# Performance work log

Measured on AMD Instinct MI355X. Metric: run time of the kernel, lower is better.

## Reference

```python
import jax, jax.numpy as jnp
import numpy as np

TAU = 5.0
ENTROPY_REG = 0.0  # entropy branch disabled (matches init kwargs)
NEG_INF = -1.0e9
NORM_EPS = 1e-12   # F.normalize eps
COS_EPS = 1e-8     # F.cosine_similarity eps


def _l2norm(x):
    n = jnp.sqrt(jnp.sum(x * x, axis=-1, keepdims=True))
    return x / jnp.maximum(n, NORM_EPS)


def setup_inputs() -> dict:
    key = jax.random.key(0)
    k1, k2, k3 = jax.random.split(key, 3)
    B, T, D = 8, 2048, 512
    pred_tokens = jax.random.normal(k1, (B, T, D), dtype=jnp.float32)
    text_tokens = jax.random.normal(k2, (B, T, D), dtype=jnp.float32)
    text_pad_mask = jax.random.randint(k3, (B, T), 0, 2).astype(jnp.bool_)  # True = PAD
    return {"pred_tokens": pred_tokens, "text_tokens": text_tokens, "text_pad_mask": text_pad_mask}


def reference(pred_tokens, text_tokens, text_pad_mask):
    B, Tp, D = pred_tokens.shape
    Tt = text_tokens.shape[1]
    T = min(Tp, Tt)
    P = _l2norm(pred_tokens[:, :T, :])            # [B,T,D]
    E = _l2norm(text_tokens[:, :T, :])            # [B,T,D]
    valid = ~text_pad_mask[:, :T]                 # [B,T] True = valid column

    S = jnp.einsum('btd,bsd->bts', P, E)          # [B,T,T]
    S = jnp.where(valid[:, None, :], S, NEG_INF)
    A = jax.nn.softmax(S * TAU, axis=-1)          # [B,T,T]
    E_hat = jnp.einsum('bts,bsd->btd', A, E)      # [B,T,D]

    # cosine similarity with eps-clamped norms (F.cosine_similarity semantics)
    dot = jnp.sum(P * E_hat, axis=-1)             # [B,T]
    pn = jnp.maximum(jnp.sqrt(jnp.sum(P * P, axis=-1)), COS_EPS)
    en = jnp.maximum(jnp.sqrt(jnp.sum(E_hat * E_hat, axis=-1)), COS_EPS)
    cos = dot / (pn * en)                         # [B,T]

    # row_has_valid: per-batch 'any valid column', broadcast over rows
    row_valid = jnp.broadcast_to(jnp.any(valid, axis=-1, keepdims=True), cos.shape)
    w = row_valid.astype(cos.dtype)
    cnt = jnp.sum(w)
    loss_sel = jnp.sum(w * (1.0 - cos)) / jnp.maximum(cnt, 1.0)
    loss = jnp.where(cnt > 0, loss_sel, jnp.zeros((), cos.dtype))
    tas = jnp.where(cnt > 0, 1.0 - jax.lax.stop_gradient(loss), loss)
    return (loss, tas)
```

## Files before the change

kernel.cpp:

```cpp
#include <hip/hip_runtime.h>
#include <cstdint>

typedef float f32x4 __attribute__((ext_vector_type(4)));
typedef long longx2 __attribute__((ext_vector_type(2)));
typedef unsigned char u8;
typedef unsigned short u16;
typedef unsigned int u32;
typedef unsigned long long u64;

#define B_N 8
#define T_N 2048
#define D_N 512
#define TAU 5.0f
#define NROW (B_N * T_N)
#define K1E 7.213475204444817f
#define K2E 1.4426950408889634f

__device__ __forceinline__ void gload_lds16(const u8* g, u8* l) {
  __builtin_amdgcn_global_load_lds(
      (const __attribute__((address_space(1))) u32*)g,
      (__attribute__((address_space(3))) u32*)l, 16, 0, 0);
}

__device__ __forceinline__ u32 pk4_fp8(float a, float b, float c, float d) {
  int w = __builtin_amdgcn_cvt_pk_fp8_f32(a, b, 0, 0);
  w = __builtin_amdgcn_cvt_pk_fp8_f32(c, d, w, 1);
  return (u32)w;
}

__device__ __forceinline__ u16 f2bf16(float x) {
  u32 u = __builtin_bit_cast(u32, x);
  u32 r = u + 0x7fffu + ((u >> 16) & 1u);
  return (u16)(r >> 16);
}
__device__ __forceinline__ float bf2f(u16 v) {
  u32 u = ((u32)v) << 16;
  return __builtin_bit_cast(float, u);
}

__global__ void kprep(const float* __restrict__ text,
                      u8* __restrict__ EF, u8* __restrict__ ET) {
  __shared__ u8 tile[32][528];
  int b = blockIdx.y, t = blockIdx.x;
  int tr = threadIdx.x;
  int row = tr >> 3, seg = tr & 7;
  const float* src = text + ((size_t)b * T_N + t * 32 + row) * D_N + seg * 64;
  float4 v[16];
  float ss = 0.f;
#pragma unroll
  for (int j = 0; j < 16; ++j) {
    v[j] = *(const float4*)(src + j * 4);
    ss += v[j].x*v[j].x + v[j].y*v[j].y + v[j].z*v[j].z + v[j].w*v[j].w;
  }
  ss += __shfl_xor(ss, 1); ss += __shfl_xor(ss, 2); ss += __shfl_xor(ss, 4);
  float inv = 1.f / fmaxf(sqrtf(ss), 1e-12f);
  u32 w[16];
#pragma unroll
  for (int j = 0; j < 16; ++j)
    w[j] = pk4_fp8(v[j].x*inv, v[j].y*inv, v[j].z*inv, v[j].w*inv);
  uint4* ldst = (uint4*)&tile[row][seg * 64];
#pragma unroll
  for (int j = 0; j < 4; ++j)
    ldst[j] = make_uint4(w[4*j], w[4*j+1], w[4*j+2], w[4*j+3]);
  __syncthreads();
  size_t tbase = ((size_t)(b * 64 + t)) << 14;
  {
    int j = tr >> 5, tok = tr & 31;
    u32 acc[16];
#pragma unroll
    for (int g2 = 0; g2 < 4; ++g2)
#pragma unroll
      for (int h = 0; h < 2; ++h) {
        uint2 vv = *(const uint2*)&tile[tok][j*64 + h*32 + g2*8];
        acc[g2*4 + h*2] = vv.x; acc[g2*4 + h*2 + 1] = vv.y;
      }
    uint4* dst = (uint4*)(EF + tbase + tr * 64);
#pragma unroll
    for (int q = 0; q < 4; ++q)
      dst[q] = make_uint4(acc[4*q], acc[4*q+1], acc[4*q+2], acc[4*q+3]);
  }
  {
    int m = tr >> 4, g2 = (tr >> 2) & 3, c0 = (tr & 3) * 4;
    u32 acc[16];
#pragma unroll
    for (int ci = 0; ci < 4; ++ci)
#pragma unroll
      for (int h = 0; h < 2; ++h) {
        int c = c0 + ci, n = 2*m + h;
        u32 lo = 0, hi = 0;
#pragma unroll
        for (int e = 0; e < 4; ++e) lo |= (u32)tile[g2*4 + e][n*16 + c] << (8*e);
#pragma unroll
        for (int e = 0; e < 4; ++e) hi |= (u32)tile[16 + g2*4 + e][n*16 + c] << (8*e);
        acc[ci*4 + h*2] = lo; acc[ci*4 + h*2 + 1] = hi;
      }
    uint4* dst = (uint4*)(ET + tbase + tr * 64);
#pragma unroll
    for (int q = 0; q < 4; ++q)
      dst[q] = make_uint4(acc[4*q], acc[4*q+1], acc[4*q+2], acc[4*q+3]);
  }
}

__launch_bounds__(256, 2)
__global__ void kflash(const float* __restrict__ pred,
                       const u8* __restrict__ EF, const u8* __restrict__ ET,
                       const int* __restrict__ mask,
                       u16* __restrict__ Opart, float* __restrict__ Lpart) {
  int b = blockIdx.x & 7;
  int rem = blockIdx.x >> 3;
  int rb = rem & 31, h = rem >> 5;
  int wid = threadIdx.x >> 6, lane = threadIdx.x & 63;
  int g = lane >> 4, c = lane & 15;
  int row0 = rb * 64 + wid * 16;
  int t0 = h * 32;

  __shared__ u64 mbits[32];
  __shared__ __align__(16) u8 els[2][16384];
  __shared__ __align__(16) u8 etls[2][16384];

  const u8* EFb = EF + (((size_t)(b * 64)) << 14) + (lane << 4);
  const u8* ETb = ET + (((size_t)(b * 64)) << 14) + (lane << 4);

  auto stage = [&](int buf, int t) {
    size_t tb = ((size_t)t) << 14;
#pragma unroll
    for (int j = 0; j < 4; ++j) {
      int ch = j * 4 + wid;
      gload_lds16(EFb + tb + (ch << 10), &els[buf][ch << 10]);
    }
#pragma unroll
    for (int j = 0; j < 4; ++j) {
      int ch = j * 4 + wid;
      gload_lds16(ETb + tb + (ch << 10), &etls[buf][ch << 10]);
    }
  };

  for (int chunk = wid; chunk < 32; chunk += 4) {
    int col = chunk * 64 + lane;
    u64 bal = __ballot(mask[b * T_N + col] == 0);
    if (lane == 0) mbits[chunk] = bal;
  }

  stage(0, t0);

  long pf[16];
  {
    int prow = row0 + c;
    const float* pr = pred + ((size_t)(b * T_N) + prow) * D_N;
    float ss = 0.f;
#pragma unroll
    for (int kk = 0; kk < 16; ++kk) {
      float4 v0 = *(const float4*)(pr + kk * 32 + g * 8);
      float4 v1 = *(const float4*)(pr + kk * 32 + g * 8 + 4);
      ss += v0.x*v0.x + v0.y*v0.y + v0.z*v0.z + v0.w*v0.w
          + v1.x*v1.x + v1.y*v1.y + v1.z*v1.z + v1.w*v1.w;
    }
    ss += __shfl_xor(ss, 16);
    ss += __shfl_xor(ss, 32);
    float inv = 1.f / fmaxf(sqrtf(ss), 1e-12f);
#pragma unroll
    for (int kk = 0; kk < 16; ++kk) {
      float4 v0 = *(const float4*)(pr + kk * 32 + g * 8);
      float4 v1 = *(const float4*)(pr + kk * 32 + g * 8 + 4);
      u32 lo = pk4_fp8(v0.x*inv, v0.y*inv, v0.z*inv, v0.w*inv);
      u32 hi = pk4_fp8(v1.x*inv, v1.y*inv, v1.z*inv, v1.w*inv);
      pf[kk] = (long)(((u64)hi << 32) | lo);
    }
  }

  __syncthreads();

  f32x4 zero = {0.f, 0.f, 0.f, 0.f};
  f32x4 eh[32];
#pragma unroll
  for (int n = 0; n < 32; ++n) eh[n] = zero;
  float lsum = 0.f;

  const int sb_off = c * 64 + g * 16;
  const int pv_off = g * 256 + c * 16;

#pragma unroll 1
  for (int tt = 0; tt < 32; ++tt) {
    int t = t0 + tt;
    int cur = tt & 1;
    if (tt + 1 < 32) stage(cur ^ 1, t + 1);
    int c0 = t * 32;

    f32x4 ta0 = zero, tb0 = zero, ta1 = zero, tb1 = zero;
    const u8* el = &els[cur][0];
    __builtin_amdgcn_s_setprio(1);
#pragma unroll
    for (int j = 0; j < 8; ++j) {
      longx2 b0 = *(const longx2*)(el + j * 2048 + sb_off);
      longx2 b1 = *(const longx2*)(el + j * 2048 + 1024 + sb_off);
      ta0 = __builtin_amdgcn_mfma_f32_16x16x32_fp8_fp8(b0[0], pf[2*j],   ta0, 0, 0, 0);
      tb0 = __builtin_amdgcn_mfma_f32_16x16x32_fp8_fp8(b0[1], pf[2*j+1], tb0, 0, 0, 0);
      ta1 = __builtin_amdgcn_mfma_f32_16x16x32_fp8_fp8(b1[0], pf[2*j],   ta1, 0, 0, 0);
      tb1 = __builtin_amdgcn_mfma_f32_16x16x32_fp8_fp8(b1[1], pf[2*j+1], tb1, 0, 0, 0);
    }
    __builtin_amdgcn_s_setprio(0);
    f32x4 st0 = ta0 + tb0, st1 = ta1 + tb1;

    u64 mw = mbits[c0 >> 6];
    u32 sh0 = (c0 & 63) + g * 4;
    u32 bits0 = (u32)(mw >> sh0) & 0xf;
    u32 bits1 = (u32)(mw >> (sh0 + 16)) & 0xf;
    float p0[4], p1[4];
#pragma unroll
    for (int r = 0; r < 4; ++r) {
      p0[r] = (bits0 >> r) & 1 ? __builtin_exp2f(fmaf(K1E, st0[r], -K2E)) : 0.f;
      p1[r] = (bits1 >> r) & 1 ? __builtin_exp2f(fmaf(K1E, st1[r], -K2E)) : 0.f;
      lsum += p0[r] + p1[r];
    }
    u32 lo = pk4_fp8(p0[0], p0[1], p0[2], p0[3]);
    u32 hi = pk4_fp8(p1[0], p1[1], p1[2], p1[3]);
    long af = (long)(((u64)hi << 32) | lo);

    const u8* et = &etls[cur][0];
    __builtin_amdgcn_s_setprio(1);
#pragma unroll
    for (int m = 0; m < 16; ++m) {
      longx2 bv = *(const longx2*)(et + m * 1024 + pv_off);
      eh[2*m]   = __builtin_amdgcn_mfma_f32_16x16x32_fp8_fp8(af, bv[0], eh[2*m],   0, 0, 0);
      eh[2*m+1] = __builtin_amdgcn_mfma_f32_16x16x32_fp8_fp8(af, bv[1], eh[2*m+1], 0, 0, 0);
    }
    __builtin_amdgcn_s_setprio(0);
    __syncthreads();
  }

  lsum += __shfl_xor(lsum, 16);
  lsum += __shfl_xor(lsum, 32);
  u16* OP = Opart + (size_t)h * ((size_t)NROW * D_N);
#pragma unroll
  for (int r = 0; r < 4; ++r) {
    int brow = b * T_N + row0 + g * 4 + r;
    u16* orow = OP + (size_t)brow * D_N + c;
#pragma unroll
    for (int n = 0; n < 32; ++n) orow[n * 16] = f2bf16(eh[n][r]);
  }
  if (g == 0) {
    Lpart[h * NROW + b * T_N + row0 + c] = lsum;
  }
}

__global__ void kcomb(const float* __restrict__ pred, const u16* __restrict__ Opart,
                      const float* __restrict__ Lpart,
                      float* __restrict__ pl, float* __restrict__ pw) {
  __shared__ float sl[8], swv[8];
  int tr = threadIdx.x;
  int row = blockIdx.x * 8 + (tr >> 5);
  int ln = tr & 31;
  float l = Lpart[row] + Lpart[NROW + row];
  const float* pr = pred + (size_t)row * D_N + ln * 16;
  const u16* o0 = Opart + (size_t)row * D_N + ln * 16;
  const u16* o1 = o0 + (size_t)NROW * D_N;
  float dot = 0.f, e2 = 0.f, pn2 = 0.f;
#pragma unroll
  for (int q = 0; q < 2; ++q) {
    uint4 a0 = *(const uint4*)(o0 + q * 8);
    uint4 a1 = *(const uint4*)(o1 + q * 8);
    u32 w0[4] = {a0.x, a0.y, a0.z, a0.w};
    u32 w1[4] = {a1.x, a1.y, a1.z, a1.w};
    float4 p0 = *(const float4*)(pr + q * 8);
    float4 p1 = *(const float4*)(pr + q * 8 + 4);
    float pp[8] = {p0.x, p0.y, p0.z, p0.w, p1.x, p1.y, p1.z, p1.w};
#pragma unroll
    for (int j = 0; j < 8; ++j) {
      float f0 = bf2f((u16)((w0[j >> 1] >> ((j & 1) * 16)) & 0xffff));
      float f1 = bf2f((u16)((w1[j >> 1] >> ((j & 1) * 16)) & 0xffff));
      float ev = f0 + f1;
      dot += pp[j] * ev;
      e2 += ev * ev;
      pn2 += pp[j] * pp[j];
    }
  }
#pragma unroll
  for (int msk = 16; msk >= 1; msk >>= 1) {
    dot += __shfl_xor(dot, msk);
    e2 += __shfl_xor(e2, msk);
    pn2 += __shfl_xor(pn2, msk);
  }
  if (ln == 0) {
    float w = (l > 0.f) ? 1.f : 0.f;
    float pn = fmaxf(sqrtf(pn2), 1e-12f);
    float denom = pn * fmaxf(sqrtf(e2), 1e-8f * l);
    float cosv = (l > 0.f) ? dot / denom : 0.f;
    sl[tr >> 5] = w * (1.f - cosv);
    swv[tr >> 5] = w;
  }
  __syncthreads();
  if (tr == 0) {
    float a = 0.f, b2 = 0.f;
#pragma unroll
    for (int i = 0; i < 8; ++i) { a += sl[i]; b2 += swv[i]; }
    pl[blockIdx.x] = a;
    pw[blockIdx.x] = b2;
  }
}

__global__ void kreduce(const float* __restrict__ pl, const float* __restrict__ pw,
                        float* __restrict__ out) {
  __shared__ float sm[256], sw[256];
  float s = 0.f, w = 0.f;
  for (int i = threadIdx.x; i < NROW / 8; i += 256) { s += pl[i]; w += pw[i]; }
  sm[threadIdx.x] = s; sw[threadIdx.x] = w;
  __syncthreads();
#pragma unroll
  for (int st = 128; st >= 1; st >>= 1) {
    if ((int)threadIdx.x < st) {
      sm[threadIdx.x] += sm[threadIdx.x + st];
      sw[threadIdx.x] += sw[threadIdx.x + st];
    }
    __syncthreads();
  }
  if (threadIdx.x == 0) {
    float cnt = sw[0];
    float loss = (cnt > 0.f) ? sm[0] / fmaxf(cnt, 1.f) : 0.f;
    out[0] = loss;
    out[1] = (cnt > 0.f) ? 1.f - loss : 0.f;
  }
}

extern "C" void kernel_launch(void* const* d_in, const int* in_sizes, int n_in,
                              void* d_out, int out_size, void* d_ws, size_t ws_size,
                              hipStream_t stream) {
  const float* pred = (const float*)d_in[0];
  const float* text = (const float*)d_in[1];
  const int* mask = (const int*)d_in[2];
  char* ws = (char*)d_ws;
  const size_t EB8 = (size_t)B_N * T_N * D_N;
  const size_t OB = (size_t)NROW * D_N * 2;
  u8* EF = (u8*)ws;
  u8* ET = (u8*)(ws + EB8);
  u16* Opart = (u16*)(ws + 2 * EB8);
  float* Lpart = (float*)(ws + 2 * EB8 + 2 * OB);
  float* pl = (float*)(ws + 2 * EB8 + 2 * OB + 131072);
  float* pw = (float*)(ws + 2 * EB8 + 2 * OB + 131072 + 16384);
  float* out = (float*)d_out;

  kprep<<<dim3(64, 8), dim3(256), 0, stream>>>(text, EF, ET);
  kflash<<<dim3(512), dim3(256), 0, stream>>>(pred, EF, ET, mask, Opart, Lpart);
  kcomb<<<dim3(NROW / 8), dim3(256), 0, stream>>>(pred, Opart, Lpart, pl, pw);
  kreduce<<<dim3(1), dim3(256), 0, stream>>>(pl, pw, out);
}
```

Measured before the change: 106.8 us.

## Load E fragments directly from global and software-pipeline S computation one tile ahead

The QK-side E tiles are no longer staged through LDS. Each lane reads its fp8 fragment directly from global memory in an MFMA-ready layout, which halves LDS footprint and staging traffic. The S=PE^T MFMAs for tile t+1 are issued before the exp/PV work of tile t, so that global load latency is overlapped. The ET staging is reordered to prefetch two tiles ahead after the barrier. The change risks exposed global-load latency and extra registers for the carried S values, which could lower occupancy.

```diff
diff --git a/kernel.cpp b/kernel.cpp
--- a/kernel.cpp
+++ b/kernel.cpp
@@ -115,19 +115,16 @@
   int t0 = h * 32;
 
   __shared__ u64 mbits[32];
-  __shared__ __align__(16) u8 els[2][16384];
   __shared__ __align__(16) u8 etls[2][16384];
 
-  const u8* EFb = EF + (((size_t)(b * 64)) << 14) + (lane << 4);
+  const int sb_off = c * 64 + g * 16;
+  const int pv_off = g * 256 + c * 16;
+
+  const u8* EFl = EF + (((size_t)(b * 64 + t0)) << 14) + sb_off;
   const u8* ETb = ET + (((size_t)(b * 64)) << 14) + (lane << 4);
 
   auto stage = [&](int buf, int t) {
     size_t tb = ((size_t)t) << 14;
-#pragma unroll
-    for (int j = 0; j < 4; ++j) {
-      int ch = j * 4 + wid;
-      gload_lds16(EFb + tb + (ch << 10), &els[buf][ch << 10]);
-    }
 #pragma unroll
     for (int j = 0; j < 4; ++j) {
       int ch = j * 4 + wid;
@@ -141,7 +138,7 @@
     if (lane == 0) mbits[chunk] = bal;
   }
 
-  stage(0, t0);
+  stage(0, t0); stage(1, t0 + 1);
 
   long pf[16];
   {
@@ -176,31 +173,31 @@
   for (int n = 0; n < 32; ++n) eh[n] = zero;
   float lsum = 0.f;
 
-  const int sb_off = c * 64 + g * 16;
-  const int pv_off = g * 256 + c * 16;
-
-#pragma unroll 1
-  for (int tt = 0; tt < 32; ++tt) {
-    int t = t0 + tt;
-    int cur = tt & 1;
-    if (tt + 1 < 32) stage(cur ^ 1, t + 1);
-    int c0 = t * 32;
-
+  auto scompute = [&](int tt, f32x4& s0, f32x4& s1) {
+    const u8* ef = EFl + ((size_t)tt << 14);
     f32x4 ta0 = zero, tb0 = zero, ta1 = zero, tb1 = zero;
-    const u8* el = &els[cur][0];
     __builtin_amdgcn_s_setprio(1);
 #pragma unroll
     for (int j = 0; j < 8; ++j) {
-      longx2 b0 = *(const longx2*)(el + j * 2048 + sb_off);
-      longx2 b1 = *(const longx2*)(el + j * 2048 + 1024 + sb_off);
+      longx2 b0 = *(const longx2*)(ef + j * 2048);
+      longx2 b1 = *(const longx2*)(ef + j * 2048 + 1024);
       ta0 = __builtin_amdgcn_mfma_f32_16x16x32_fp8_fp8(b0[0], pf[2*j],   ta0, 0, 0, 0);
       tb0 = __builtin_amdgcn_mfma_f32_16x16x32_fp8_fp8(b0[1], pf[2*j+1], tb0, 0, 0, 0);
       ta1 = __builtin_amdgcn_mfma_f32_16x16x32_fp8_fp8(b1[0], pf[2*j],   ta1, 0, 0, 0);
       tb1 = __builtin_amdgcn_mfma_f32_16x16x32_fp8_fp8(b1[1], pf[2*j+1], tb1, 0, 0, 0);
     }
     __builtin_amdgcn_s_setprio(0);
-    f32x4 st0 = ta0 + tb0, st1 = ta1 + tb1;
-
+    s0 = ta0 + tb0; s1 = ta1 + tb1;
+  };
+
+  f32x4 s0c, s1c, s0n, s1n;
+  scompute(0, s0c, s1c);
+
+#pragma unroll 1
+  for (int tt = 0; tt < 32; ++tt) {
+    if (tt + 1 < 32) scompute(tt + 1, s0n, s1n);
+
+    int c0 = (t0 + tt) * 32;
     u64 mw = mbits[c0 >> 6];
     u32 sh0 = (c0 & 63) + g * 4;
     u32 bits0 = (u32)(mw >> sh0) & 0xf;
@@ -208,15 +205,15 @@
     float p0[4], p1[4];
 #pragma unroll
     for (int r = 0; r < 4; ++r) {
-      p0[r] = (bits0 >> r) & 1 ? __builtin_exp2f(fmaf(K1E, st0[r], -K2E)) : 0.f;
-      p1[r] = (bits1 >> r) & 1 ? __builtin_exp2f(fmaf(K1E, st1[r], -K2E)) : 0.f;
+      p0[r] = (bits0 >> r) & 1 ? __builtin_exp2f(fmaf(K1E, s0c[r], -K2E)) : 0.f;
+      p1[r] = (bits1 >> r) & 1 ? __builtin_exp2f(fmaf(K1E, s1c[r], -K2E)) : 0.f;
       lsum += p0[r] + p1[r];
     }
     u32 lo = pk4_fp8(p0[0], p0[1], p0[2], p0[3]);
     u32 hi = pk4_fp8(p1[0], p1[1], p1[2], p1[3]);
     long af = (long)(((u64)hi << 32) | lo);
 
-    const u8* et = &etls[cur][0];
+    const u8* et = &etls[tt & 1][0];
     __builtin_amdgcn_s_setprio(1);
 #pragma unroll
     for (int m = 0; m < 16; ++m) {
@@ -226,6 +223,8 @@
     }
     __builtin_amdgcn_s_setprio(0);
     __syncthreads();
+    if (tt < 30) stage(tt & 1, t0 + tt + 2);
+    s0c = s0n; s1c = s1n;
   }
 
   lsum += __shfl_xor(lsum, 16);
```

Measured after the change: 151.3 us. 41.7% more time.

## Double flash block size, split staging with fine-grained barriers, fold dot product into softmax

Applied to the files above, without the earlier changes.

The attention kernel now runs 512-thread blocks covering 128 rows, so every staged E tile is shared by twice as many waves and half as many blocks reload it. The per-step staging is split into separate E and ET loads, each guarded by explicit vmcnt waits and mid-loop barriers, so loads for the next steps are issued while the current MFMAs run. The dot product P·E_hat is rebuilt inside the flash loop as the sum of p*s, which lets the combine kernel skip reading pred entirely. In exchange there are more barriers per iteration, higher register and LDS pressure per block, and the dot is now computed from fp8-quantized scores.

```diff
diff --git a/kernel.cpp b/kernel.cpp
--- a/kernel.cpp
+++ b/kernel.cpp
@@ -15,6 +15,9 @@
 #define NROW (B_N * T_N)
 #define K1E 7.213475204444817f
 #define K2E 1.4426950408889634f
+
+#define WAITV(n) asm volatile("s_waitcnt vmcnt(" #n ")" ::: "memory")
+#define BAR      __builtin_amdgcn_s_barrier()
 
 __device__ __forceinline__ void gload_lds16(const u8* g, u8* l) {
   __builtin_amdgcn_global_load_lds(
@@ -101,17 +104,18 @@
   }
 }
 
-__launch_bounds__(256, 2)
+__launch_bounds__(512, 2)
 __global__ void kflash(const float* __restrict__ pred,
                        const u8* __restrict__ EF, const u8* __restrict__ ET,
                        const int* __restrict__ mask,
-                       u16* __restrict__ Opart, float* __restrict__ Lpart) {
+                       u16* __restrict__ Opart, float* __restrict__ Lpart,
+                       float* __restrict__ Dpart) {
   int b = blockIdx.x & 7;
   int rem = blockIdx.x >> 3;
-  int rb = rem & 31, h = rem >> 5;
+  int rb = rem & 15, h = rem >> 4;
   int wid = threadIdx.x >> 6, lane = threadIdx.x & 63;
   int g = lane >> 4, c = lane & 15;
-  int row0 = rb * 64 + wid * 16;
+  int row0 = rb * 128 + wid * 16;
   int t0 = h * 32;
 
   __shared__ u64 mbits[32];
@@ -121,27 +125,30 @@
   const u8* EFb = EF + (((size_t)(b * 64)) << 14) + (lane << 4);
   const u8* ETb = ET + (((size_t)(b * 64)) << 14) + (lane << 4);
 
-  auto stage = [&](int buf, int t) {
+  auto stageE = [&](int buf, int t) {
     size_t tb = ((size_t)t) << 14;
 #pragma unroll
-    for (int j = 0; j < 4; ++j) {
-      int ch = j * 4 + wid;
+    for (int j = 0; j < 2; ++j) {
+      int ch = wid * 2 + j;
       gload_lds16(EFb + tb + (ch << 10), &els[buf][ch << 10]);
     }
-#pragma unroll
-    for (int j = 0; j < 4; ++j) {
-      int ch = j * 4 + wid;
+  };
+  auto stageET = [&](int buf, int t) {
+    size_t tb = ((size_t)t) << 14;
+#pragma unroll
+    for (int j = 0; j < 2; ++j) {
+      int ch = wid * 2 + j;
       gload_lds16(ETb + tb + (ch << 10), &etls[buf][ch << 10]);
     }
   };
 
-  for (int chunk = wid; chunk < 32; chunk += 4) {
+  for (int chunk = wid; chunk < 32; chunk += 8) {
     int col = chunk * 64 + lane;
     u64 bal = __ballot(mask[b * T_N + col] == 0);
     if (lane == 0) mbits[chunk] = bal;
   }
 
-  stage(0, t0);
+  stageE(0, t0); stageET(0, t0); stageE(1, t0 + 1);
 
   long pf[16];
   {
@@ -174,23 +181,23 @@
   f32x4 eh[32];
 #pragma unroll
   for (int n = 0; n < 32; ++n) eh[n] = zero;
-  float lsum = 0.f;
+  float lsum = 0.f, dsum = 0.f;
 
   const int sb_off = c * 64 + g * 16;
   const int pv_off = g * 256 + c * 16;
 
 #pragma unroll 1
   for (int tt = 0; tt < 32; ++tt) {
-    int t = t0 + tt;
     int cur = tt & 1;
-    if (tt + 1 < 32) stage(cur ^ 1, t + 1);
-    int c0 = t * 32;
-
+    if (tt < 31) { WAITV(2); } else { WAITV(0); }
+    BAR;
+
+    if (tt < 31) stageET(cur ^ 1, t0 + tt + 1);
+    const u8* el = &els[cur][0];
     f32x4 ta0 = zero, tb0 = zero, ta1 = zero, tb1 = zero;
-    const u8* el = &els[cur][0];
     __builtin_amdgcn_s_setprio(1);
 #pragma unroll
-    for (int j = 0; j < 8; ++j) {
+    for (int j = 0; j < 4; ++j) {
       longx2 b0 = *(const longx2*)(el + j * 2048 + sb_off);
       longx2 b1 = *(const longx2*)(el + j * 2048 + 1024 + sb_off);
       ta0 = __builtin_amdgcn_mfma_f32_16x16x32_fp8_fp8(b0[0], pf[2*j],   ta0, 0, 0, 0);
@@ -199,8 +206,24 @@
       tb1 = __builtin_amdgcn_mfma_f32_16x16x32_fp8_fp8(b1[1], pf[2*j+1], tb1, 0, 0, 0);
     }
     __builtin_amdgcn_s_setprio(0);
+    BAR;
+
+    __builtin_amdgcn_s_setprio(1);
+#pragma unroll
+    for (int j = 4; j < 8; ++j) {
+      longx2 b0 = *(const longx2*)(el + j * 2048 + sb_off);
+      longx2 b1 = *(const longx2*)(el + j * 2048 + 1024 + sb_off);
+      ta0 = __builtin_amdgcn_mfma_f32_16x16x32_fp8_fp8(b0[0], pf[2*j],   ta0, 0, 0, 0);
+      tb0 = __builtin_amdgcn_mfma_f32_16x16x32_fp8_fp8(b0[1], pf[2*j+1], tb0, 0, 0, 0);
+      ta1 = __builtin_amdgcn_mfma_f32_16x16x32_fp8_fp8(b1[0], pf[2*j],   ta1, 0, 0, 0);
+      tb1 = __builtin_amdgcn_mfma_f32_16x16x32_fp8_fp8(b1[1], pf[2*j+1], tb1, 0, 0, 0);
+    }
+    __builtin_amdgcn_s_setprio(0);
     f32x4 st0 = ta0 + tb0, st1 = ta1 + tb1;
-
+    BAR;
+
+    if (tt < 30) stageE(cur, t0 + tt + 2);
+    int c0 = (t0 + tt) * 32;
     u64 mw = mbits[c0 >> 6];
     u32 sh0 = (c0 & 63) + g * 4;
     u32 bits0 = (u32)(mw >> sh0) & 0xf;
@@ -211,6 +234,7 @@
       p0[r] = (bits0 >> r) & 1 ? __builtin_exp2f(fmaf(K1E, st0[r], -K2E)) : 0.f;
       p1[r] = (bits1 >> r) & 1 ? __builtin_exp2f(fmaf(K1E, st1[r], -K2E)) : 0.f;
       lsum += p0[r] + p1[r];
+      dsum += p0[r] * st0[r] + p1[r] * st1[r];
     }
     u32 lo = pk4_fp8(p0[0], p0[1], p0[2], p0[3]);
     u32 hi = pk4_fp8(p1[0], p1[1], p1[2], p1[3]);
@@ -219,17 +243,28 @@
     const u8* et = &etls[cur][0];
     __builtin_amdgcn_s_setprio(1);
 #pragma unroll
-    for (int m = 0; m < 16; ++m) {
+    for (int m = 0; m < 8; ++m) {
       longx2 bv = *(const longx2*)(et + m * 1024 + pv_off);
       eh[2*m]   = __builtin_amdgcn_mfma_f32_16x16x32_fp8_fp8(af, bv[0], eh[2*m],   0, 0, 0);
       eh[2*m+1] = __builtin_amdgcn_mfma_f32_16x16x32_fp8_fp8(af, bv[1], eh[2*m+1], 0, 0, 0);
     }
     __builtin_amdgcn_s_setprio(0);
-    __syncthreads();
+    BAR;
+
+    __builtin_amdgcn_s_setprio(1);
+#pragma unroll
+    for (int m = 8; m < 16; ++m) {
+      longx2 bv = *(const longx2*)(et + m * 1024 + pv_off);
+      eh[2*m]   = __builtin_amdgcn_mfma_f32_16x16x32_fp8_fp8(af, bv[0], eh[2*m],   0, 0, 0);
+      eh[2*m+1] = __builtin_amdgcn_mfma_f32_16x16x32_fp8_fp8(af, bv[1], eh[2*m+1], 0, 0, 0);
+    }
+    __builtin_amdgcn_s_setprio(0);
   }
 
   lsum += __shfl_xor(lsum, 16);
   lsum += __shfl_xor(lsum, 32);
+  dsum += __shfl_xor(dsum, 16);
+  dsum += __shfl_xor(dsum, 32);
   u16* OP = Opart + (size_t)h * ((size_t)NROW * D_N);
 #pragma unroll
   for (int r = 0; r < 4; ++r) {
@@ -240,51 +275,41 @@
   }
   if (g == 0) {
     Lpart[h * NROW + b * T_N + row0 + c] = lsum;
-  }
-}
-
-__global__ void kcomb(const float* __restrict__ pred, const u16* __restrict__ Opart,
-                      const float* __restrict__ Lpart,
+    Dpart[h * NROW + b * T_N + row0 + c] = dsum;
+  }
+}
+
+__global__ void kcomb(const u16* __restrict__ Opart, const float* __restrict__ Lpart,
+                      const float* __restrict__ Dpart,
                       float* __restrict__ pl, float* __restrict__ pw) {
   __shared__ float sl[8], swv[8];
   int tr = threadIdx.x;
   int row = blockIdx.x * 8 + (tr >> 5);
   int ln = tr & 31;
   float l = Lpart[row] + Lpart[NROW + row];
-  const float* pr = pred + (size_t)row * D_N + ln * 16;
+  float dot = Dpart[row] + Dpart[NROW + row];
   const u16* o0 = Opart + (size_t)row * D_N + ln * 16;
   const u16* o1 = o0 + (size_t)NROW * D_N;
-  float dot = 0.f, e2 = 0.f, pn2 = 0.f;
+  float e2 = 0.f;
 #pragma unroll
   for (int q = 0; q < 2; ++q) {
     uint4 a0 = *(const uint4*)(o0 + q * 8);
     uint4 a1 = *(const uint4*)(o1 + q * 8);
     u32 w0[4] = {a0.x, a0.y, a0.z, a0.w};
     u32 w1[4] = {a1.x, a1.y, a1.z, a1.w};
-    float4 p0 = *(const float4*)(pr + q * 8);
-    float4 p1 = *(const float4*)(pr + q * 8 + 4);
-    float pp[8] = {p0.x, p0.y, p0.z, p0.w, p1.x, p1.y, p1.z, p1.w};
 #pragma unroll
     for (int j = 0; j < 8; ++j) {
       float f0 = bf2f((u16)((w0[j >> 1] >> ((j & 1) * 16)) & 0xffff));
       float f1 = bf2f((u16)((w1[j >> 1] >> ((j & 1) * 16)) & 0xffff));
       float ev = f0 + f1;
-      dot += pp[j] * ev;
       e2 += ev * ev;
-      pn2 += pp[j] * pp[j];
-    }
-  }
-#pragma unroll
-  for (int msk = 16; msk >= 1; msk >>= 1) {
-    dot += __shfl_xor(dot, msk);
-    e2 += __shfl_xor(e2, msk);
-    pn2 += __shfl_xor(pn2, msk);
-  }
+    }
+  }
+#pragma unroll
+  for (int msk = 16; msk >= 1; msk >>= 1) e2 += __shfl_xor(e2, msk);
   if (ln == 0) {
     float w = (l > 0.f) ? 1.f : 0.f;
-    float pn = fmaxf(sqrtf(pn2), 1e-12f);
-    float denom = pn * fmaxf(sqrtf(e2), 1e-8f * l);
-    float cosv = (l > 0.f) ? dot / denom : 0.f;
+    float cosv = (l > 0.f) ? dot / fmaxf(sqrtf(e2), 1e-8f * l) : 0.f;
     sl[tr >> 5] = w * (1.f - cosv);
     swv[tr >> 5] = w;
   }
@@ -333,13 +358,15 @@
   u8* EF = (u8*)ws;
   u8* ET = (u8*)(ws + EB8);
   u16* Opart = (u16*)(ws + 2 * EB8);
-  float* Lpart = (float*)(ws + 2 * EB8 + 2 * OB);
-  float* pl = (float*)(ws + 2 * EB8 + 2 * OB + 131072);
-  float* pw = (float*)(ws + 2 * EB8 + 2 * OB + 131072 + 16384);
+  char* base2 = ws + 2 * EB8 + 2 * OB;
+  float* Lpart = (float*)(base2);
+  float* Dpart = (float*)(base2 + 131072);
+  float* pl = (float*)(base2 + 262144);
+  float* pw = (float*)(base2 + 262144 + 16384);
   float* out = (float*)d_out;
 
   kprep<<<dim3(64, 8), dim3(256), 0, stream>>>(text, EF, ET);
-  kflash<<<dim3(512), dim3(256), 0, stream>>>(pred, EF, ET, mask, Opart, Lpart);
-  kcomb<<<dim3(NROW / 8), dim3(256), 0, stream>>>(pred, Opart, Lpart, pl, pw);
+  kflash<<<dim3(256), dim3(512), 0, stream>>>(pred, EF, ET, mask, Opart, Lpart, Dpart);
+  kcomb<<<dim3(NROW / 8), dim3(256), 0, stream>>>(Opart, Lpart, Dpart, pl, pw);
   kreduce<<<dim3(1), dim3(256), 0, stream>>>(pl, pw, out);
 }
```

Result: faster. 103.5 us (-3.1%).
